# Kernel tuning notes

Hardware: AMD Instinct MI355X
Metric: run time of the kernel (lower is better)

Reference implementation:

```python
import jax, jax.numpy as jnp
import numpy as np

N = 100000   # nodes
D = 64       # in_features == out_features
E = 1600000  # edges (avg degree 16)
C = 1.0      # curvature
MIN_NORM = 1e-15
PROJ_EPS = 1e-5
ATANH_CLIP = 1.0 - 1e-7


def _artanh(x):
    return jnp.arctanh(jnp.clip(x, -ATANH_CLIP, ATANH_CLIP))


def _norm(x):
    return jnp.clip(jnp.linalg.norm(x, axis=-1, keepdims=True), MIN_NORM)


def setup_inputs() -> dict:
    key = jax.random.key(0)
    k1, k2, k3, k4, k5 = jax.random.split(key, 5)
    # points inside the unit ball (module assumes input already on manifold)
    x = 0.05 * jax.random.normal(k1, (N, D), dtype=jnp.float32)
    # xavier_uniform with gain sqrt(2): std ~= sqrt(2)*sqrt(2/(D+D))
    W = jax.random.normal(k2, (D, D), dtype=jnp.float32) * np.float32(np.sqrt(4.0 / (2 * D)))
    edge_vals = jax.random.uniform(k3, (E,), dtype=jnp.float32) / 16.0  # ~normalized adjacency
    rows = jax.random.randint(k4, (E,), 0, N, dtype=jnp.int32)
    cols = jax.random.randint(k5, (E,), 0, N, dtype=jnp.int32)
    return {"x": x, "W": W, "edge_vals": edge_vals, "rows": rows, "cols": cols}


def reference(x, W, edge_vals, rows, cols):
    sc = jnp.sqrt(jnp.float32(C))
    # --- Poincare Linear: mobius_matvec(W, x, c) (no bias, eval-mode dropout) ---
    mx = x @ W.T                                  # [N, D]
    x_n = _norm(x)
    mx_n = _norm(mx)
    res = jnp.tanh(mx_n / x_n * _artanh(sc * x_n)) * mx / (mx_n * sc)
    res = jnp.where(jnp.all(mx == 0, axis=-1, keepdims=True), 0.0, res)
    # --- poincare2euclidean == logmap0 ---
    p_n = _norm(res)
    hidden = _artanh(sc * p_n) * res / (sc * p_n)  # tangent at origin
    # --- sparse adjacency matmul: support = adj @ hidden ---
    gathered = edge_vals[:, None] * hidden[cols]   # [E, D]
    support = jax.ops.segment_sum(gathered, rows, num_segments=N)
    # --- euclidean2poincare == expmap0 ---
    u_n = _norm(support)
    p = jnp.tanh(sc * u_n) * support / (sc * u_n)
    # --- Act: relu(logmap0) -> proj_tan0 (identity) -> expmap0 -> proj ---
    pn2 = _norm(p)
    xt = jax.nn.relu(_artanh(sc * pn2) * p / (sc * pn2))
    xt_n = _norm(xt)
    out = jnp.tanh(sc * xt_n) * xt / (sc * xt_n)
    o_n = _norm(out)
    max_n = (1.0 - PROJ_EPS) / sc
    out = jnp.where(o_n > max_n, out / o_n * max_n, out)
    return out
```

## Files before the change

kernel.cpp:

```cpp
#include <hip/hip_runtime.h>
#include <hip/hip_fp16.h>

#define NN 100000
#define DD 64
#define EE 1600000
#define NB 512
#define NPB 196
#define NPAD (NB * NPB)
#define CHUNK 3125
#define SORT_BLOCKS 512
#define CAP 3520
#define LIN_BLOCKS 1567

typedef _Float16 half8 __attribute__((ext_vector_type(8)));
typedef float floatx4 __attribute__((ext_vector_type(4)));

__device__ __forceinline__ float frcp(float x) { return __builtin_amdgcn_rcpf(x); }

__device__ __forceinline__ float fast_tanh(float x) {
    float t = __expf(2.0f * x);
    return (t - 1.0f) * frcp(t + 1.0f);
}
__device__ __forceinline__ float fast_atanh(float x) {
    const float CLIP = 1.0f - 1e-7f;
    x = fminf(fmaxf(x, -CLIP), CLIP);
    return 0.5f * __logf((1.0f + x) * frcp(1.0f - x));
}
__device__ __forceinline__ float group16_reduce_sum(float v) {
    #pragma unroll
    for (int m = 8; m > 0; m >>= 1) v += __shfl_xor(v, m, 16);
    return v;
}
__device__ __forceinline__ float lo16f(unsigned u) {
    return __half2float(__ushort_as_half((unsigned short)(u & 0xFFFFu)));
}
__device__ __forceinline__ float hi16f(unsigned u) {
    return __half2float(__ushort_as_half((unsigned short)(u >> 16)));
}

__global__ __launch_bounds__(256) void linear_kernel(
    const float* __restrict__ x, const float* __restrict__ W,
    __half* __restrict__ hidden) {
    __shared__ _Float16 Wh[64 * 80];
    const int t = threadIdx.x;
    for (int i = t; i < 64 * 64; i += 256)
        Wh[(i >> 6) * 80 + (i & 63)] = (_Float16)W[i];
    __syncthreads();

    const int lane = t & 63;
    const int wv   = t >> 6;
    const int q    = lane >> 4;
    const int c    = lane & 15;
    const int node = (blockIdx.x * 4 + wv) * 16 + c;
    const int node_ld = (node < NN) ? node : (NN - 1);

    const float MIN_NORM = 1e-15f;
    const float4* xr = (const float4*)(x + node_ld * 64);
    float4 b0a = xr[q * 2];
    float4 b0b = xr[q * 2 + 1];
    float4 b1a = xr[8 + q * 2];
    float4 b1b = xr[8 + q * 2 + 1];

    float xpart = b0a.x*b0a.x + b0a.y*b0a.y + b0a.z*b0a.z + b0a.w*b0a.w
                + b0b.x*b0b.x + b0b.y*b0b.y + b0b.z*b0b.z + b0b.w*b0b.w
                + b1a.x*b1a.x + b1a.y*b1a.y + b1a.z*b1a.z + b1a.w*b1a.w
                + b1b.x*b1b.x + b1b.y*b1b.y + b1b.z*b1b.z + b1b.w*b1b.w;
    xpart += __shfl_xor(xpart, 16, 64);
    xpart += __shfl_xor(xpart, 32, 64);
    float x_n = fmaxf(sqrtf(xpart), MIN_NORM);

    half8 bf0, bf1;
    bf0[0]=(_Float16)b0a.x; bf0[1]=(_Float16)b0a.y; bf0[2]=(_Float16)b0a.z; bf0[3]=(_Float16)b0a.w;
    bf0[4]=(_Float16)b0b.x; bf0[5]=(_Float16)b0b.y; bf0[6]=(_Float16)b0b.z; bf0[7]=(_Float16)b0b.w;
    bf1[0]=(_Float16)b1a.x; bf1[1]=(_Float16)b1a.y; bf1[2]=(_Float16)b1a.z; bf1[3]=(_Float16)b1a.w;
    bf1[4]=(_Float16)b1b.x; bf1[5]=(_Float16)b1b.y; bf1[6]=(_Float16)b1b.z; bf1[7]=(_Float16)b1b.w;

    floatx4 acc[4];
    #pragma unroll
    for (int tt = 0; tt < 4; ++tt) {
        const half8* a0 = (const half8*)&Wh[(16 * tt + c) * 80 + q * 8];
        const half8* a1 = (const half8*)&Wh[(16 * tt + c) * 80 + 32 + q * 8];
        floatx4 z = {0.f, 0.f, 0.f, 0.f};
        z = __builtin_amdgcn_mfma_f32_16x16x32_f16(a0[0], bf0, z, 0, 0, 0);
        z = __builtin_amdgcn_mfma_f32_16x16x32_f16(a1[0], bf1, z, 0, 0, 0);
        acc[tt] = z;
    }

    float hscale = fast_atanh(x_n) * frcp(x_n);

    if (node < NN) {
        #pragma unroll
        for (int tt = 0; tt < 4; ++tt) {
            __half2 lo = __floats2half2_rn(acc[tt][0] * hscale, acc[tt][1] * hscale);
            __half2 hi = __floats2half2_rn(acc[tt][2] * hscale, acc[tt][3] * hscale);
            uint2 pkt;
            pkt.x = *(unsigned*)&lo;
            pkt.y = *(unsigned*)&hi;
            ((uint2*)hidden)[node * 16 + tt * 4 + q] = pkt;
        }
    }
}

__global__ __launch_bounds__(1024) void count_kernel(const int* __restrict__ rows,
                                                     int* __restrict__ cnt) {
    __shared__ int h[NB];
    const int t  = threadIdx.x;
    const int e0 = blockIdx.x * CHUNK;
    if (t < NB) h[t] = 0;
    __syncthreads();
    for (int i = t; i < CHUNK; i += 1024)
        atomicAdd(&h[(unsigned)rows[e0 + i] / NPB], 1);
    __syncthreads();
    if (t < NB) cnt[blockIdx.x * NB + t] = h[t];
}

__global__ __launch_bounds__(512) void offset_kernel(int* __restrict__ cnt,
                                                     int* __restrict__ gcount) {
    const int lane = threadIdx.x & 63;
    const int b    = blockIdx.x * 8 + (threadIdx.x >> 6);
    int c[8]; int sum = 0;
    #pragma unroll
    for (int k = 0; k < 8; ++k) { c[k] = cnt[(lane * 8 + k) * NB + b]; sum += c[k]; }
    int pre = sum;
    #pragma unroll
    for (int m = 1; m < 64; m <<= 1) {
        int u = __shfl_up(pre, m, 64);
        if (lane >= m) pre += u;
    }
    int run = pre - sum;
    #pragma unroll
    for (int k = 0; k < 8; ++k) { cnt[(lane * 8 + k) * NB + b] = run; run += c[k]; }
    if (lane == 63) gcount[b] = run;
}

__global__ __launch_bounds__(64) void scan_kernel(const int* __restrict__ gcount,
                                                  int* __restrict__ bbase) {
    const int lane = threadIdx.x;
    int c[8]; int sum = 0;
    #pragma unroll
    for (int k = 0; k < 8; ++k) { c[k] = gcount[lane * 8 + k]; sum += c[k]; }
    int pre = sum;
    #pragma unroll
    for (int m = 1; m < 64; m <<= 1) {
        int u = __shfl_up(pre, m, 64);
        if (lane >= m) pre += u;
    }
    int run = pre - sum;
    #pragma unroll
    for (int k = 0; k < 8; ++k) { bbase[lane * 8 + k] = run; run += c[k]; }
    if (lane == 63) bbase[NB] = run;
}

__global__ __launch_bounds__(1024) void sort_scatter_kernel(
    const int* __restrict__ rows, const int* __restrict__ cols,
    const float* __restrict__ ev, const int* __restrict__ woff,
    const int* __restrict__ bbase, int2* __restrict__ csr) {
    __shared__ int hist[NB];
    __shared__ int offs[NB];
    __shared__ int delta[NB];
    __shared__ int2 sorted[CHUNK];
    __shared__ unsigned short bid[CHUNK];
    const int t  = threadIdx.x;
    const int e0 = blockIdx.x * CHUNK;

    if (t < NB) hist[t] = 0;
    __syncthreads();
    for (int i = t; i < CHUNK; i += 1024)
        atomicAdd(&hist[(unsigned)rows[e0 + i] / NPB], 1);
    __syncthreads();
    if (t < 64) {
        const int lane = t;
        int c[8]; int sum = 0;
        #pragma unroll
        for (int k = 0; k < 8; ++k) { c[k] = hist[lane * 8 + k]; sum += c[k]; }
        int pre = sum;
        #pragma unroll
        for (int m = 1; m < 64; m <<= 1) {
            int u = __shfl_up(pre, m, 64);
            if (lane >= m) pre += u;
        }
        int run = pre - sum;
        #pragma unroll
        for (int k = 0; k < 8; ++k) {
            int b = lane * 8 + k;
            offs[b]  = run;
            delta[b] = bbase[b] + woff[blockIdx.x * NB + b] - run;
            hist[b]  = 0;
            run += c[k];
        }
    }
    __syncthreads();
    for (int i = t; i < CHUNK; i += 1024) {
        unsigned r = (unsigned)rows[e0 + i];
        unsigned c = (unsigned)cols[e0 + i];
        float v = ev[e0 + i];
        unsigned b  = r / NPB;
        unsigned rl = r - b * NPB;
        int pos = atomicAdd(&hist[b], 1);
        int idx = offs[b] + pos;
        sorted[idx] = make_int2((int)((rl << 24) | (c << 7)), __float_as_int(v));
        bid[idx] = (unsigned short)b;
    }
    __syncthreads();
    for (int i = t; i < CHUNK; i += 1024) {
        int2 eV = sorted[i];
        csr[delta[bid[i]] + i] = eV;
    }
}

__global__ __launch_bounds__(1024) void sortgather_kernel(
    const __half* __restrict__ hidden, const int2* __restrict__ csr,
    const int* __restrict__ bbase, float* __restrict__ out) {
    __shared__ int2 srt[CAP];
    __shared__ int cnt_a[NPB];
    __shared__ int start[NPB];
    __shared__ int cur[NPB];
    const int t  = threadIdx.x;
    const int b  = blockIdx.x;
    const int lo = bbase[b];
    int cnt = bbase[b + 1] - lo;
    if (cnt > CAP) cnt = CAP;

    if (t < NPB) cnt_a[t] = 0;
    __syncthreads();
    for (int i = t; i < cnt; i += 1024)
        atomicAdd(&cnt_a[((unsigned)csr[lo + i].x) >> 24], 1);
    __syncthreads();
    if (t < 64) {
        const int lane = t;
        int c[4]; int sum = 0;
        #pragma unroll
        for (int k = 0; k < 4; ++k) {
            int bb = lane * 4 + k;
            c[k] = (bb < NPB) ? cnt_a[bb] : 0;
            sum += c[k];
        }
        int pre = sum;
        #pragma unroll
        for (int m = 1; m < 64; m <<= 1) {
            int u = __shfl_up(pre, m, 64);
            if (lane >= m) pre += u;
        }
        int run = pre - sum;
        #pragma unroll
        for (int k = 0; k < 4; ++k) {
            int bb = lane * 4 + k;
            if (bb < NPB) { start[bb] = run; cur[bb] = run; run += c[k]; }
        }
    }
    __syncthreads();
    for (int i = t; i < cnt; i += 1024) {
        int2 e = csr[lo + i];
        int rl = ((unsigned)e.x) >> 24;
        int p  = atomicAdd(&cur[rl], 1);
        srt[p] = e;
    }
    __syncthreads();

    const int lane = t & 63;
    const int wv   = t >> 6;
    const int g    = lane >> 4;
    const int l8   = (lane & 15) * 8;
    const char* __restrict__ hidc = (const char*)hidden;
    const float MIN_NORM = 1e-15f;
    const float MAX_N = 1.0f - 1e-5f;

    for (int n = wv; n < NPB; n += 16) {
        int i   = start[n];
        int rhi = i + cnt_a[n];
        float ax = 0.f, ay = 0.f, az = 0.f, aw = 0.f;

        for (; i + 8 <= rhi; i += 8) {
            int2 dA = srt[i + g];
            int2 dB = srt[i + 4 + g];
            unsigned oA = (((unsigned)dA.x) & 0xFFFFFFu) + l8;
            unsigned oB = (((unsigned)dB.x) & 0xFFFFFFu) + l8;
            uint2 hA = *(const uint2*)(hidc + oA);
            uint2 hB = *(const uint2*)(hidc + oB);
            float vA = __int_as_float(dA.y);
            float vB = __int_as_float(dB.y);
            ax = fmaf(vA, lo16f(hA.x), ax);
            ay = fmaf(vA, hi16f(hA.x), ay);
            az = fmaf(vA, lo16f(hA.y), az);
            aw = fmaf(vA, hi16f(hA.y), aw);
            ax = fmaf(vB, lo16f(hB.x), ax);
            ay = fmaf(vB, hi16f(hB.x), ay);
            az = fmaf(vB, lo16f(hB.y), az);
            aw = fmaf(vB, hi16f(hB.y), aw);
        }
        for (; i < rhi; i += 4) {
            int idx = i + g;
            int2 d = srt[(idx < rhi) ? idx : (rhi - 1)];
            float v = (idx < rhi) ? __int_as_float(d.y) : 0.0f;
            unsigned o = (((unsigned)d.x) & 0xFFFFFFu) + l8;
            uint2 h = *(const uint2*)(hidc + o);
            ax = fmaf(v, lo16f(h.x), ax);
            ay = fmaf(v, hi16f(h.x), ay);
            az = fmaf(v, lo16f(h.y), az);
            aw = fmaf(v, hi16f(h.y), aw);
        }

        ax += __shfl_xor(ax, 16, 64); ax += __shfl_xor(ax, 32, 64);
        ay += __shfl_xor(ay, 16, 64); ay += __shfl_xor(ay, 32, 64);
        az += __shfl_xor(az, 16, 64); az += __shfl_xor(az, 32, 64);
        aw += __shfl_xor(aw, 16, 64); aw += __shfl_xor(aw, 32, 64);

        float xx = fmaxf(ax, 0.f), xy = fmaxf(ay, 0.f);
        float xz = fmaxf(az, 0.f), xw = fmaxf(aw, 0.f);

        float part = xx*xx + xy*xy + xz*xz + xw*xw;
        float xt_n = fmaxf(sqrtf(group16_reduce_sum(part)), MIN_NORM);
        float txt  = fast_tanh(xt_n);
        float s3   = txt * frcp(xt_n);
        if (txt > MAX_N) s3 = MAX_N * frcp(xt_n);
        float ox = xx*s3, oy = xy*s3, oz = xz*s3, ow = xw*s3;

        int gn = b * NPB + n;
        if (g == 0 && gn < NN) {
            float4 o4 = make_float4(ox, oy, oz, ow);
            *(float4*)(out + gn * DD + (lane & 15) * 4) = o4;
        }
    }
}

extern "C" void kernel_launch(void* const* d_in, const int* in_sizes, int n_in,
                              void* d_out, int out_size, void* d_ws, size_t ws_size,
                              hipStream_t stream) {
    const float* x    = (const float*)d_in[0];
    const float* W    = (const float*)d_in[1];
    const float* ev   = (const float*)d_in[2];
    const int*   rows = (const int*)d_in[3];
    const int*   cols = (const int*)d_in[4];
    float* out = (float*)d_out;

    char* ws = (char*)d_ws;
    __half* hidden = (__half*)ws;
    int2*   csr    = (int2*)(ws + 12800000);
    int*    cnt    = (int*)(ws + 25600000);
    int*    gcount = (int*)(ws + 26648576);
    int*    bbase  = (int*)(ws + 26650624);

    linear_kernel<<<LIN_BLOCKS, 256, 0, stream>>>(x, W, hidden);
    count_kernel<<<SORT_BLOCKS, 1024, 0, stream>>>(rows, cnt);
    offset_kernel<<<NB / 8, 512, 0, stream>>>(cnt, gcount);
    scan_kernel<<<1, 64, 0, stream>>>(gcount, bbase);
    sort_scatter_kernel<<<SORT_BLOCKS, 1024, 0, stream>>>(rows, cols, ev, cnt, bbase, csr);
    sortgather_kernel<<<NB, 1024, 0, stream>>>(hidden, csr, bbase, out);
}
```

Before: 150.4 us.

## Fuse linear transform with row-bucket counting and reuse counts in scatter

The Poincaré linear transform and the per-chunk row-bucket histogram are merged into one 512-block kernel of 1024 threads. Each block counts one edge chunk and processes 196 nodes, using 13 waves for the MFMA work. The offset kernel now writes its prefix offsets to a separate buffer, so the scatter kernel can read the saved per-chunk counts instead of building the histogram again. This removes one kernel launch and one redundant pass over the rows array, at the cost of leaving 3 of 16 waves idle during the linear part.

```diff
diff --git a/kernel.cpp b/kernel.cpp
--- a/kernel.cpp
+++ b/kernel.cpp
@@ -6,11 +6,8 @@
 #define EE 1600000
 #define NB 512
 #define NPB 196
-#define NPAD (NB * NPB)
 #define CHUNK 3125
-#define SORT_BLOCKS 512
 #define CAP 3520
-#define LIN_BLOCKS 1567
 
 typedef _Float16 half8 __attribute__((ext_vector_type(8)));
 typedef float floatx4 __attribute__((ext_vector_type(4)));
@@ -38,83 +35,85 @@
     return __half2float(__ushort_as_half((unsigned short)(u >> 16)));
 }
 
-__global__ __launch_bounds__(256) void linear_kernel(
+__global__ __launch_bounds__(1024) void linear_count_kernel(
     const float* __restrict__ x, const float* __restrict__ W,
-    __half* __restrict__ hidden) {
+    const int* __restrict__ rows,
+    __half* __restrict__ hidden, int* __restrict__ cnt) {
     __shared__ _Float16 Wh[64 * 80];
+    __shared__ int h[NB];
     const int t = threadIdx.x;
-    for (int i = t; i < 64 * 64; i += 256)
+
+    if (t < NB) h[t] = 0;
+    for (int i = t; i < 64 * 64; i += 1024)
         Wh[(i >> 6) * 80 + (i & 63)] = (_Float16)W[i];
     __syncthreads();
+
+    {
+        const int e0 = blockIdx.x * CHUNK;
+        for (int i = t; i < CHUNK; i += 1024)
+            atomicAdd(&h[(unsigned)rows[e0 + i] / NPB], 1);
+    }
 
     const int lane = t & 63;
     const int wv   = t >> 6;
-    const int q    = lane >> 4;
-    const int c    = lane & 15;
-    const int node = (blockIdx.x * 4 + wv) * 16 + c;
-    const int node_ld = (node < NN) ? node : (NN - 1);
-
-    const float MIN_NORM = 1e-15f;
-    const float4* xr = (const float4*)(x + node_ld * 64);
-    float4 b0a = xr[q * 2];
-    float4 b0b = xr[q * 2 + 1];
-    float4 b1a = xr[8 + q * 2];
-    float4 b1b = xr[8 + q * 2 + 1];
-
-    float xpart = b0a.x*b0a.x + b0a.y*b0a.y + b0a.z*b0a.z + b0a.w*b0a.w
-                + b0b.x*b0b.x + b0b.y*b0b.y + b0b.z*b0b.z + b0b.w*b0b.w
-                + b1a.x*b1a.x + b1a.y*b1a.y + b1a.z*b1a.z + b1a.w*b1a.w
-                + b1b.x*b1b.x + b1b.y*b1b.y + b1b.z*b1b.z + b1b.w*b1b.w;
-    xpart += __shfl_xor(xpart, 16, 64);
-    xpart += __shfl_xor(xpart, 32, 64);
-    float x_n = fmaxf(sqrtf(xpart), MIN_NORM);
-
-    half8 bf0, bf1;
-    bf0[0]=(_Float16)b0a.x; bf0[1]=(_Float16)b0a.y; bf0[2]=(_Float16)b0a.z; bf0[3]=(_Float16)b0a.w;
-    bf0[4]=(_Float16)b0b.x; bf0[5]=(_Float16)b0b.y; bf0[6]=(_Float16)b0b.z; bf0[7]=(_Float16)b0b.w;
-    bf1[0]=(_Float16)b1a.x; bf1[1]=(_Float16)b1a.y; bf1[2]=(_Float16)b1a.z; bf1[3]=(_Float16)b1a.w;
-    bf1[4]=(_Float16)b1b.x; bf1[5]=(_Float16)b1b.y; bf1[6]=(_Float16)b1b.z; bf1[7]=(_Float16)b1b.w;
-
-    floatx4 acc[4];
-    #pragma unroll
-    for (int tt = 0; tt < 4; ++tt) {
-        const half8* a0 = (const half8*)&Wh[(16 * tt + c) * 80 + q * 8];
-        const half8* a1 = (const half8*)&Wh[(16 * tt + c) * 80 + 32 + q * 8];
-        floatx4 z = {0.f, 0.f, 0.f, 0.f};
-        z = __builtin_amdgcn_mfma_f32_16x16x32_f16(a0[0], bf0, z, 0, 0, 0);
-        z = __builtin_amdgcn_mfma_f32_16x16x32_f16(a1[0], bf1, z, 0, 0, 0);
-        acc[tt] = z;
-    }
-
-    float hscale = fast_atanh(x_n) * frcp(x_n);
-
-    if (node < NN) {
+    if (wv < 13) {
+        const int q    = lane >> 4;
+        const int c    = lane & 15;
+        const int node = blockIdx.x * NPB + wv * 16 + c;
+        const int node_ld = (node < NN) ? node : (NN - 1);
+
+        const float MIN_NORM = 1e-15f;
+        const float4* xr = (const float4*)(x + node_ld * 64);
+        float4 b0a = xr[q * 2];
+        float4 b0b = xr[q * 2 + 1];
+        float4 b1a = xr[8 + q * 2];
+        float4 b1b = xr[8 + q * 2 + 1];
+
+        float xpart = b0a.x*b0a.x + b0a.y*b0a.y + b0a.z*b0a.z + b0a.w*b0a.w
+                    + b0b.x*b0b.x + b0b.y*b0b.y + b0b.z*b0b.z + b0b.w*b0b.w
+                    + b1a.x*b1a.x + b1a.y*b1a.y + b1a.z*b1a.z + b1a.w*b1a.w
+                    + b1b.x*b1b.x + b1b.y*b1b.y + b1b.z*b1b.z + b1b.w*b1b.w;
+        xpart += __shfl_xor(xpart, 16, 64);
+        xpart += __shfl_xor(xpart, 32, 64);
+        float x_n = fmaxf(sqrtf(xpart), MIN_NORM);
+
+        half8 bf0, bf1;
+        bf0[0]=(_Float16)b0a.x; bf0[1]=(_Float16)b0a.y; bf0[2]=(_Float16)b0a.z; bf0[3]=(_Float16)b0a.w;
+        bf0[4]=(_Float16)b0b.x; bf0[5]=(_Float16)b0b.y; bf0[6]=(_Float16)b0b.z; bf0[7]=(_Float16)b0b.w;
+        bf1[0]=(_Float16)b1a.x; bf1[1]=(_Float16)b1a.y; bf1[2]=(_Float16)b1a.z; bf1[3]=(_Float16)b1a.w;
+        bf1[4]=(_Float16)b1b.x; bf1[5]=(_Float16)b1b.y; bf1[6]=(_Float16)b1b.z; bf1[7]=(_Float16)b1b.w;
+
+        floatx4 acc[4];
         #pragma unroll
         for (int tt = 0; tt < 4; ++tt) {
-            __half2 lo = __floats2half2_rn(acc[tt][0] * hscale, acc[tt][1] * hscale);
-            __half2 hi = __floats2half2_rn(acc[tt][2] * hscale, acc[tt][3] * hscale);
-            uint2 pkt;
-            pkt.x = *(unsigned*)&lo;
-            pkt.y = *(unsigned*)&hi;
-            ((uint2*)hidden)[node * 16 + tt * 4 + q] = pkt;
-        }
-    }
-}
-
-__global__ __launch_bounds__(1024) void count_kernel(const int* __restrict__ rows,
-                                                     int* __restrict__ cnt) {
-    __shared__ int h[NB];
-    const int t  = threadIdx.x;
-    const int e0 = blockIdx.x * CHUNK;
-    if (t < NB) h[t] = 0;
-    __syncthreads();
-    for (int i = t; i < CHUNK; i += 1024)
-        atomicAdd(&h[(unsigned)rows[e0 + i] / NPB], 1);
+            const half8* a0 = (const half8*)&Wh[(16 * tt + c) * 80 + q * 8];
+            const half8* a1 = (const half8*)&Wh[(16 * tt + c) * 80 + 32 + q * 8];
+            floatx4 z = {0.f, 0.f, 0.f, 0.f};
+            z = __builtin_amdgcn_mfma_f32_16x16x32_f16(a0[0], bf0, z, 0, 0, 0);
+            z = __builtin_amdgcn_mfma_f32_16x16x32_f16(a1[0], bf1, z, 0, 0, 0);
+            acc[tt] = z;
+        }
+
+        float hscale = fast_atanh(x_n) * frcp(x_n);
+
+        if (node < NN) {
+            #pragma unroll
+            for (int tt = 0; tt < 4; ++tt) {
+                __half2 lo = __floats2half2_rn(acc[tt][0] * hscale, acc[tt][1] * hscale);
+                __half2 hi = __floats2half2_rn(acc[tt][2] * hscale, acc[tt][3] * hscale);
+                uint2 pkt;
+                pkt.x = *(unsigned*)&lo;
+                pkt.y = *(unsigned*)&hi;
+                ((uint2*)hidden)[node * 16 + tt * 4 + q] = pkt;
+            }
+        }
+    }
     __syncthreads();
     if (t < NB) cnt[blockIdx.x * NB + t] = h[t];
 }
 
-__global__ __launch_bounds__(512) void offset_kernel(int* __restrict__ cnt,
+__global__ __launch_bounds__(512) void offset_kernel(const int* __restrict__ cnt,
+                                                     int* __restrict__ woff,
                                                      int* __restrict__ gcount) {
     const int lane = threadIdx.x & 63;
     const int b    = blockIdx.x * 8 + (threadIdx.x >> 6);
@@ -129,7 +128,7 @@
     }
     int run = pre - sum;
     #pragma unroll
-    for (int k = 0; k < 8; ++k) { cnt[(lane * 8 + k) * NB + b] = run; run += c[k]; }
+    for (int k = 0; k < 8; ++k) { woff[(lane * 8 + k) * NB + b] = run; run += c[k]; }
     if (lane == 63) gcount[b] = run;
 }
 
@@ -153,26 +152,21 @@
 
 __global__ __launch_bounds__(1024) void sort_scatter_kernel(
     const int* __restrict__ rows, const int* __restrict__ cols,
-    const float* __restrict__ ev, const int* __restrict__ woff,
-    const int* __restrict__ bbase, int2* __restrict__ csr) {
-    __shared__ int hist[NB];
-    __shared__ int offs[NB];
+    const float* __restrict__ ev, const int* __restrict__ cnt,
+    const int* __restrict__ woff, const int* __restrict__ bbase,
+    int2* __restrict__ csr) {
+    __shared__ int cur[NB];
     __shared__ int delta[NB];
     __shared__ int2 sorted[CHUNK];
     __shared__ unsigned short bid[CHUNK];
     const int t  = threadIdx.x;
     const int e0 = blockIdx.x * CHUNK;
 
-    if (t < NB) hist[t] = 0;
-    __syncthreads();
-    for (int i = t; i < CHUNK; i += 1024)
-        atomicAdd(&hist[(unsigned)rows[e0 + i] / NPB], 1);
-    __syncthreads();
     if (t < 64) {
         const int lane = t;
         int c[8]; int sum = 0;
         #pragma unroll
-        for (int k = 0; k < 8; ++k) { c[k] = hist[lane * 8 + k]; sum += c[k]; }
+        for (int k = 0; k < 8; ++k) { c[k] = cnt[blockIdx.x * NB + lane * 8 + k]; sum += c[k]; }
         int pre = sum;
         #pragma unroll
         for (int m = 1; m < 64; m <<= 1) {
@@ -183,9 +177,8 @@
         #pragma unroll
         for (int k = 0; k < 8; ++k) {
             int b = lane * 8 + k;
-            offs[b]  = run;
+            cur[b]   = run;
             delta[b] = bbase[b] + woff[blockIdx.x * NB + b] - run;
-            hist[b]  = 0;
             run += c[k];
         }
     }
@@ -196,8 +189,7 @@
         float v = ev[e0 + i];
         unsigned b  = r / NPB;
         unsigned rl = r - b * NPB;
-        int pos = atomicAdd(&hist[b], 1);
-        int idx = offs[b] + pos;
+        int idx = atomicAdd(&cur[b], 1);
         sorted[idx] = make_int2((int)((rl << 24) | (c << 7)), __float_as_int(v));
         bid[idx] = (unsigned short)b;
     }
@@ -337,13 +329,13 @@
     __half* hidden = (__half*)ws;
     int2*   csr    = (int2*)(ws + 12800000);
     int*    cnt    = (int*)(ws + 25600000);
-    int*    gcount = (int*)(ws + 26648576);
-    int*    bbase  = (int*)(ws + 26650624);
-
-    linear_kernel<<<LIN_BLOCKS, 256, 0, stream>>>(x, W, hidden);
-    count_kernel<<<SORT_BLOCKS, 1024, 0, stream>>>(rows, cnt);
-    offset_kernel<<<NB / 8, 512, 0, stream>>>(cnt, gcount);
+    int*    woff   = (int*)(ws + 26648576);
+    int*    gcount = (int*)(ws + 27697152);
+    int*    bbase  = (int*)(ws + 27699200);
+
+    linear_count_kernel<<<NB, 1024, 0, stream>>>(x, W, rows, hidden, cnt);
+    offset_kernel<<<NB / 8, 512, 0, stream>>>(cnt, woff, gcount);
     scan_kernel<<<1, 64, 0, stream>>>(gcount, bbase);
-    sort_scatter_kernel<<<SORT_BLOCKS, 1024, 0, stream>>>(rows, cols, ev, cnt, bbase, csr);
+    sort_scatter_kernel<<<NB, 1024, 0, stream>>>(rows, cols, ev, cnt, woff, bbase, csr);
     sortgather_kernel<<<NB, 1024, 0, stream>>>(hidden, csr, bbase, out);
 }
```

Measured after the change: 149.4 us (median of 2 runs). About the same (-0.6%).
